# Kernel tuning notes

Measured on AMD Instinct MI355X. Metric: run time of the kernel, lower is better.

## Reference

```python
import jax, jax.numpy as jnp
import numpy as np

B, OH, OW = 64, 120, 160
THRESHOLD = 0.5


def setup_inputs() -> dict:
    key = jax.random.key(0)
    k1, k2, k3, k4 = jax.random.split(key, 4)
    return {
        'heatmap': jax.random.uniform(k1, (B, 1, OH, OW), dtype=jnp.float32),
        'scale': jax.random.uniform(k2, (B, 2, OH, OW), dtype=jnp.float32),
        'offset': jax.random.uniform(k3, (B, 2, OH, OW), dtype=jnp.float32),
        'landmark': jax.random.uniform(k4, (B, 10, OH, OW), dtype=jnp.float32),
    }


def reference(heatmap, scale, offset, landmark):
    batch, _, out_h, out_w = heatmap.shape
    in_h = jnp.float32(out_h * 4)
    in_w = jnp.float32(out_w * 4)

    s0 = jnp.exp(scale[:, 0]) * 4.0   # [B,H,W]
    s1 = jnp.exp(scale[:, 1]) * 4.0
    o0 = offset[:, 0]
    o1 = offset[:, 1]

    my = jnp.arange(out_h, dtype=jnp.float32)[None, :, None]   # broadcast grid y
    # NOTE: original torch code overwrites x1 with maximum(y1, 0) (a bug we replicate):
    # the x-grid/o1 term is dead code.
    y1_raw = (my + o0 + 0.5) * 4.0 - s0 / 2.0
    y1c = jnp.maximum(y1_raw, 0.0)
    y1 = jnp.minimum(y1c, in_h)
    x1 = jnp.minimum(y1c, in_w)   # faithful to the torch bug

    y2 = jnp.minimum(y1 + s0, in_h)
    x2 = jnp.minimum(x1 + s1, in_w)
    s = heatmap[:, 0]  # [B,H,W]

    hw = out_h * out_w
    all_boxes = jnp.stack([x1, y1, x2, y2, s], axis=-1).reshape(batch, hw, 5)

    lm = jnp.transpose(landmark, (0, 2, 3, 1)).reshape(batch, hw, 10)
    s0r = s0.reshape(batch, hw, 1)
    s1r = s1.reshape(batch, hw, 1)
    y1r = y1.reshape(batch, hw, 1)
    x1r = x1.reshape(batch, hw, 1)
    lm_y = lm[:, :, 0::2] * s0r + y1r   # [B,HW,5]
    lm_x = lm[:, :, 1::2] * s1r + x1r   # [B,HW,5]
    landmark_yx = jnp.stack([lm_y, lm_x], axis=-1).reshape(batch, hw, 10)

    # The torch code does data-dependent boolean indexing; for fixed shapes we
    # zero out rows below threshold and also return the keep mask.
    keep = all_boxes[:, :, 4] >= THRESHOLD  # [B,HW]
    boxes_out = jnp.where(keep[:, :, None], all_boxes, 0.0)
    landmarks_out = jnp.where(keep[:, :, None], landmark_yx, 0.0)
    return boxes_out, landmarks_out, keep
```

## Files before the change

### kernel.cpp

```cpp
#include <hip/hip_runtime.h>

#define OW_   160
#define OH_   120
#define HW_   (OH_ * OW_)
#define BATCH 64
#define NPIX  (BATCH * HW_)
#define BLK   256

#define BOX_OFF 0
#define LM_OFF  ((size_t)NPIX * 5)
#define KEEP_OFF ((size_t)NPIX * 15)

__global__ __launch_bounds__(BLK) void detpost_kernel(
    const float* __restrict__ heatmap,
    const float* __restrict__ scale,
    const float* __restrict__ offset,
    const float* __restrict__ landmark,
    float* __restrict__ boxes,
    float* __restrict__ lms,
    float* __restrict__ keepo)
{
    __shared__ float sbox[BLK * 5];
    __shared__ float slm [BLK * 10];

    const int tid = threadIdx.x;
    const int idx = blockIdx.x * BLK + tid;
    const int b   = idx / HW_;
    const int p   = idx - b * HW_;
    const int h   = p / OW_;

    const float s    = heatmap[idx];
    const float* scb = scale  + (size_t)b * 2 * HW_;
    const float sc0  = scb[p];
    const float sc1  = scb[HW_ + p];
    const float off0 = offset[(size_t)b * 2 * HW_ + p];

    const float s0 = __expf(sc0) * 4.0f;
    const float s1 = __expf(sc1) * 4.0f;
    const float y1raw = ((float)h + off0 + 0.5f) * 4.0f - s0 * 0.5f;
    const float y1c = fmaxf(y1raw, 0.0f);
    const float y1  = fminf(y1c, 480.0f);
    const float x1  = fminf(y1c, 640.0f);
    const float y2  = fminf(y1 + s0, 480.0f);
    const float x2  = fminf(x1 + s1, 640.0f);

    const bool keep = (s >= 0.5f);

    sbox[tid * 5 + 0] = keep ? x1 : 0.0f;
    sbox[tid * 5 + 1] = keep ? y1 : 0.0f;
    sbox[tid * 5 + 2] = keep ? x2 : 0.0f;
    sbox[tid * 5 + 3] = keep ? y2 : 0.0f;
    sbox[tid * 5 + 4] = keep ? s  : 0.0f;

    const float* lmb = landmark + (size_t)b * 10 * HW_ + p;
#pragma unroll
    for (int c = 0; c < 10; ++c) {
        const float lv = lmb[(size_t)c * HW_];
        const float v  = (c & 1) ? fmaf(lv, s1, x1) : fmaf(lv, s0, y1);
        slm[tid * 10 + c] = keep ? v : 0.0f;
    }

    keepo[idx] = keep ? 1.0f : 0.0f;

    __syncthreads();

    {
        const float4* sb4 = (const float4*)sbox;
        float4* gb4 = (float4*)(boxes + (size_t)blockIdx.x * (BLK * 5));
#pragma unroll
        for (int j = tid; j < BLK * 5 / 4; j += BLK) gb4[j] = sb4[j];
    }
    {
        const float4* sl4 = (const float4*)slm;
        float4* gl4 = (float4*)(lms + (size_t)blockIdx.x * (BLK * 10));
#pragma unroll
        for (int j = tid; j < BLK * 10 / 4; j += BLK) gl4[j] = sl4[j];
    }
}

extern "C" void kernel_launch(void* const* d_in, const int* in_sizes, int n_in,
                              void* d_out, int out_size, void* d_ws, size_t ws_size,
                              hipStream_t stream) {
    const float* heatmap  = (const float*)d_in[0];
    const float* scale    = (const float*)d_in[1];
    const float* offset   = (const float*)d_in[2];
    const float* landmark = (const float*)d_in[3];

    float* out   = (float*)d_out;
    float* boxes = out + BOX_OFF;
    float* lms   = out + LM_OFF;
    float* keepo = out + KEEP_OFF;

    const int nblocks = NPIX / BLK;
    detpost_kernel<<<nblocks, BLK, 0, stream>>>(heatmap, scale, offset, landmark,
                                                boxes, lms, keepo);
}
```

Measured before the change: 139.8 us.

## Process two pixels per thread with vectorized loads and nontemporal stores

```diff
diff --git a/kernel.cpp b/kernel.cpp
--- a/kernel.cpp
+++ b/kernel.cpp
@@ -6,10 +6,15 @@
 #define BATCH 64
 #define NPIX  (BATCH * HW_)
 #define BLK   256
+#define PPT   2
+#define PPB   (BLK * PPT)
 
 #define BOX_OFF 0
 #define LM_OFF  ((size_t)NPIX * 5)
 #define KEEP_OFF ((size_t)NPIX * 15)
+
+typedef float f2v __attribute__((ext_vector_type(2)));
+typedef float f4v __attribute__((ext_vector_type(4)));
 
 __global__ __launch_bounds__(BLK) void detpost_kernel(
     const float* __restrict__ heatmap,
@@ -20,61 +25,85 @@
     float* __restrict__ lms,
     float* __restrict__ keepo)
 {
-    __shared__ float sbox[BLK * 5];
-    __shared__ float slm [BLK * 10];
+    __shared__ float sbox[PPB * 5];
+    __shared__ float slm [PPB * 10];
 
-    const int tid = threadIdx.x;
-    const int idx = blockIdx.x * BLK + tid;
-    const int b   = idx / HW_;
-    const int p   = idx - b * HW_;
-    const int h   = p / OW_;
+    const int tid  = threadIdx.x;
+    const int gp   = blockIdx.x * BLK + tid;
+    const int base = gp * 2;
+    const int b    = base / HW_;
+    const int p    = base - b * HW_;
+    const int h    = p / OW_;
 
-    const float s    = heatmap[idx];
-    const float* scb = scale  + (size_t)b * 2 * HW_;
-    const float sc0  = scb[p];
-    const float sc1  = scb[HW_ + p];
-    const float off0 = offset[(size_t)b * 2 * HW_ + p];
-
-    const float s0 = __expf(sc0) * 4.0f;
-    const float s1 = __expf(sc1) * 4.0f;
-    const float y1raw = ((float)h + off0 + 0.5f) * 4.0f - s0 * 0.5f;
-    const float y1c = fmaxf(y1raw, 0.0f);
-    const float y1  = fminf(y1c, 480.0f);
-    const float x1  = fminf(y1c, 640.0f);
-    const float y2  = fminf(y1 + s0, 480.0f);
-    const float x2  = fminf(x1 + s1, 640.0f);
-
-    const bool keep = (s >= 0.5f);
-
-    sbox[tid * 5 + 0] = keep ? x1 : 0.0f;
-    sbox[tid * 5 + 1] = keep ? y1 : 0.0f;
-    sbox[tid * 5 + 2] = keep ? x2 : 0.0f;
-    sbox[tid * 5 + 3] = keep ? y2 : 0.0f;
-    sbox[tid * 5 + 4] = keep ? s  : 0.0f;
+    const f2v hm   = *(const f2v*)(heatmap + base);
+    const float* scb = scale + (size_t)b * 2 * HW_;
+    const f2v sc0v = *(const f2v*)(scb + p);
+    const f2v sc1v = *(const f2v*)(scb + HW_ + p);
+    const f2v of0v = *(const f2v*)(offset + (size_t)b * 2 * HW_ + p);
 
     const float* lmb = landmark + (size_t)b * 10 * HW_ + p;
+    f2v lmv[10];
+#pragma unroll
+    for (int c = 0; c < 10; ++c) lmv[c] = *(const f2v*)(lmb + (size_t)c * HW_);
+
+    float s0a[2], s1a[2], y1a[2], x1a[2];
+    bool  kp[2];
+    f2v   kk;
+#pragma unroll
+    for (int q = 0; q < 2; ++q) {
+        const float sc  = q ? hm.y   : hm.x;
+        const float sc0 = q ? sc0v.y : sc0v.x;
+        const float sc1 = q ? sc1v.y : sc1v.x;
+        const float o0  = q ? of0v.y : of0v.x;
+
+        const float s0 = __expf(sc0) * 4.0f;
+        const float s1 = __expf(sc1) * 4.0f;
+        const float y1raw = ((float)h + o0 + 0.5f) * 4.0f - s0 * 0.5f;
+        const float y1c = fmaxf(y1raw, 0.0f);
+        const float y1  = fminf(y1c, 480.0f);
+        const float x1  = fminf(y1c, 640.0f);
+        const float y2  = fminf(y1 + s0, 480.0f);
+        const float x2  = fminf(x1 + s1, 640.0f);
+        const bool keep = (sc >= 0.5f);
+
+        float* sb = sbox + (2 * tid + q) * 5;
+        sb[0] = keep ? x1 : 0.0f;
+        sb[1] = keep ? y1 : 0.0f;
+        sb[2] = keep ? x2 : 0.0f;
+        sb[3] = keep ? y2 : 0.0f;
+        sb[4] = keep ? sc : 0.0f;
+
+        s0a[q] = s0; s1a[q] = s1; y1a[q] = y1; x1a[q] = x1; kp[q] = keep;
+        if (q == 0) kk.x = keep ? 1.0f : 0.0f; else kk.y = keep ? 1.0f : 0.0f;
+    }
+
 #pragma unroll
     for (int c = 0; c < 10; ++c) {
-        const float lv = lmb[(size_t)c * HW_];
-        const float v  = (c & 1) ? fmaf(lv, s1, x1) : fmaf(lv, s0, y1);
-        slm[tid * 10 + c] = keep ? v : 0.0f;
+#pragma unroll
+        for (int q = 0; q < 2; ++q) {
+            const float lv = q ? lmv[c].y : lmv[c].x;
+            const float v  = (c & 1) ? fmaf(lv, s1a[q], x1a[q]) : fmaf(lv, s0a[q], y1a[q]);
+            slm[(2 * tid + q) * 10 + c] = kp[q] ? v : 0.0f;
+        }
     }
 
-    keepo[idx] = keep ? 1.0f : 0.0f;
+    __builtin_nontemporal_store(kk, (f2v*)(keepo + base));
 
     __syncthreads();
 
     {
-        const float4* sb4 = (const float4*)sbox;
-        float4* gb4 = (float4*)(boxes + (size_t)blockIdx.x * (BLK * 5));
+        const f4v* sb4 = (const f4v*)sbox;
+        f4v* gb4 = (f4v*)(boxes + (size_t)blockIdx.x * (PPB * 5));
 #pragma unroll
-        for (int j = tid; j < BLK * 5 / 4; j += BLK) gb4[j] = sb4[j];
+        for (int j = tid; j < PPB * 5 / 4; j += BLK)
+            __builtin_nontemporal_store(sb4[j], gb4 + j);
     }
     {
-        const float4* sl4 = (const float4*)slm;
-        float4* gl4 = (float4*)(lms + (size_t)blockIdx.x * (BLK * 10));
+        const f4v* sl4 = (const f4v*)slm;
+        f4v* gl4 = (f4v*)(lms + (size_t)blockIdx.x * (PPB * 10));
 #pragma unroll
-        for (int j = tid; j < BLK * 10 / 4; j += BLK) gl4[j] = sl4[j];
+        for (int j = tid; j < PPB * 10 / 4; j += BLK)
+            __builtin_nontemporal_store(sl4[j], gl4 + j);
     }
 }
 
@@ -91,7 +120,7 @@
     float* lms   = out + LM_OFF;
     float* keepo = out + KEEP_OFF;
 
-    const int nblocks = NPIX / BLK;
+    const int nblocks = NPIX / PPB;
     detpost_kernel<<<nblocks, BLK, 0, stream>>>(heatmap, scale, offset, landmark,
                                                 boxes, lms, keepo);
 }
```

Result: no change. 138.3 us (-1.1%).
